# Performance work log

Measured on AMD Instinct MI355X. Metric: run time of the kernel, lower is better.

Reference implementation:

```python
import jax, jax.numpy as jnp
import numpy as np

EPS = 1e-5

def ln(x, g, b):
    m = x.mean(-1, keepdims=True)
    v = ((x - m) ** 2).mean(-1, keepdims=True)
    return (x - m) / jnp.sqrt(v + EPS) * g + b

def mha(x, in_w, in_b, out_w, out_b, nh):
    # Faithful nn.MultiheadAttention with batch_first=False: x is (L, B, D),
    # attention runs over axis 0 (sequence), axis 1 is batch.
    L, Bb, D = x.shape
    hd = D // nh
    qkv = x @ in_w.T + in_b                      # (L, B, 3D)
    q, k, v = jnp.split(qkv, 3, axis=-1)
    q = q.reshape(L, Bb, nh, hd) * (hd ** -0.5)
    k = k.reshape(L, Bb, nh, hd)
    v = v.reshape(L, Bb, nh, hd)
    a = jax.nn.softmax(jnp.einsum('lbhe,sbhe->bhls', q, k), axis=-1)
    o = jnp.einsum('bhls,sbhe->lbhe', a, v).reshape(L, Bb, D)
    return o @ out_w.T + out_b

def psb_forward(features, prev_slots,
                lnq_g, lnq_b, lnkv_g, lnkv_b,
                wq, wk, wv, wo,
                lnt_g, lnt_b, t_in_w, t_in_b, t_out_w, t_out_b,
                lno_g, lno_b, o_in_w, o_in_b, o_out_w, o_out_b,
                lnp_g, lnp_b, w1, b1, w2, b2):
    B, T, L, D = features.shape
    N = prev_slots.shape[2]
    nh = 1                                        # inverse_nh
    hd = D // nh
    slots = ln(prev_slots, lnq_g, lnq_b).reshape(B * T, N, D)
    xkv = ln(features, lnkv_g, lnkv_b).reshape(B * T, L, D)
    # ---- inverse cross attention (softmax over query/slot dim, renorm over keys) ----
    q = (slots @ wq.T).reshape(B * T, N, nh, hd).transpose(0, 2, 1, 3) * (D ** -0.5)
    k = (xkv @ wk.T).reshape(B * T, L, nh, hd).transpose(0, 2, 1, 3)
    v = (xkv @ wv.T).reshape(B * T, L, nh, hd).transpose(0, 2, 1, 3)
    attn = jnp.einsum('bhnd,bhsd->bhns', q, k)    # (BT, nh, N, L)
    attn = jax.nn.softmax(attn, axis=-2)          # over slots (queries)
    attn = attn / attn.sum(-1, keepdims=True)     # renormalize over keys
    s = jnp.einsum('bhns,bhsd->bnhd', attn, v).reshape(B * T, N, D) @ wo.T
    # ---- time attention: input (B*T, N, D); seq axis 0 = B*T, batch = N ----
    s = ln(s, lnt_g, lnt_b)
    s = mha(s, t_in_w, t_in_b, t_out_w, t_out_b, 4)
    # rearrange '(b t) n d -> (b n) t d'
    s = s.reshape(B, T, N, D).transpose(0, 2, 1, 3).reshape(B * N, T, D)
    # ---- object attention: seq axis 0 = B*N, batch = T ----
    s = ln(s, lno_g, lno_b)
    s = mha(s, o_in_w, o_in_b, o_out_w, o_out_b, 4)
    # faithful to torch .view(B, T, N, D) on a contiguous (B*N, T, D) tensor:
    # raw row-major reinterpretation (same as torch)
    s = s.reshape(B, T, N, D)
    # ---- FFN projection + residual with prev_slots ----
    s = ln(s, lnp_g, lnp_b)
    s = jax.nn.relu(s @ w1.T + b1) @ w2.T + b2
    return s + prev_slots

def setup_inputs() -> dict:
    key = jax.random.key(0)
    ks = jax.random.split(key, 16)
    B, T, L, D, N, F = 8, 16, 1024, 192, 8, 512
    w = lambda k, shape: jax.random.normal(k, shape, jnp.float32) * 0.02
    return {
        'features': jax.random.normal(ks[0], (B, T, L, D), jnp.float32),
        'prev_slots': jax.random.normal(ks[1], (B, T, N, D), jnp.float32),
        'lnq_g': jnp.ones((D,), jnp.float32), 'lnq_b': jnp.zeros((D,), jnp.float32),
        'lnkv_g': jnp.ones((D,), jnp.float32), 'lnkv_b': jnp.zeros((D,), jnp.float32),
        'wq': w(ks[2], (D, D)), 'wk': w(ks[3], (D, D)),
        'wv': w(ks[4], (D, D)), 'wo': w(ks[5], (D, D)),
        'lnt_g': jnp.ones((D,), jnp.float32), 'lnt_b': jnp.zeros((D,), jnp.float32),
        't_in_w': w(ks[6], (3 * D, D)), 't_in_b': jnp.zeros((3 * D,), jnp.float32),
        't_out_w': w(ks[7], (D, D)), 't_out_b': jnp.zeros((D,), jnp.float32),
        'lno_g': jnp.ones((D,), jnp.float32), 'lno_b': jnp.zeros((D,), jnp.float32),
        'o_in_w': w(ks[8], (3 * D, D)), 'o_in_b': jnp.zeros((3 * D,), jnp.float32),
        'o_out_w': w(ks[9], (D, D)), 'o_out_b': jnp.zeros((D,), jnp.float32),
        'lnp_g': jnp.ones((D,), jnp.float32), 'lnp_b': jnp.zeros((D,), jnp.float32),
        'w1': w(ks[10], (F, D)), 'b1': jnp.zeros((F,), jnp.float32),
        'w2': w(ks[11], (D, F)), 'b2': jnp.zeros((D,), jnp.float32),
    }

def reference(features, prev_slots,
              lnq_g, lnq_b, lnkv_g, lnkv_b,
              wq, wk, wv, wo,
              lnt_g, lnt_b, t_in_w, t_in_b, t_out_w, t_out_b,
              lno_g, lno_b, o_in_w, o_in_b, o_out_w, o_out_b,
              lnp_g, lnp_b, w1, b1, w2, b2):
    return psb_forward(features, prev_slots,
                       lnq_g, lnq_b, lnkv_g, lnkv_b,
                       wq, wk, wv, wo,
                       lnt_g, lnt_b, t_in_w, t_in_b, t_out_w, t_out_b,
                       lno_g, lno_b, o_in_w, o_in_b, o_out_w, o_out_b,
                       lnp_g, lnp_b, w1, b1, w2, b2)
```

## Files before the change

kernel.cpp:

```cpp
#include <hip/hip_runtime.h>
#include <hip/hip_bf16.h>
#include <stdint.h>

typedef __hip_bfloat16 bf16;

__device__ __forceinline__ float b2f(bf16 x){ return __bfloat162float(x); }
__device__ __forceinline__ bf16  f2b(float x){ return __float2bfloat16(x); }
__device__ __forceinline__ float bfl(unsigned u){ return __uint_as_float(u << 16); }
__device__ __forceinline__ float bfh(unsigned u){ return __uint_as_float(u & 0xffff0000u); }
__device__ __forceinline__ int dflag(const void* rawg){
  return *(const uint32_t*)rawg == 0x3F803F80u;
}

struct Ptrs26 { const void* p[26]; };
__global__ __launch_bounds__(256) void k_convert(Ptrs26 ps, float* __restrict__ dst){
  constexpr int kN[26] = {192,192,192,192, 36864,36864,36864,36864, 192,192,
                          110592,576, 36864,192, 192,192, 110592,576, 36864,192,
                          192,192, 98304,512, 98304,192};
  constexpr int kR[26] = {0,0,0,0, 0,0,0,0, 0,0,
                          576,0, 192,0, 0,0, 576,0, 192,0,
                          0,0, 512,0, 192,0};
  const int b = blockIdx.x;
  int tz = 0, boff = 0, off = 0;
  for (int i = 0; i < 26; ++i){
    const int nb = (kN[i] + 255) >> 8;
    if (b < boff + nb){ tz = i; break; }
    boff += nb; off += kN[i];
  }
  const int cnt = kN[tz];
  const int tid = (b - boff)*256 + threadIdx.x;
  if (tid >= cnt) return;
  const int flag = dflag(ps.p[0]);
  float v = flag ? b2f(((const bf16*)ps.p[tz])[tid]) : ((const float*)ps.p[tz])[tid];
  const int R = kR[tz];
  if (R == 0){
    dst[off + tid] = v;
  } else {
    const int K = cnt / R;
    int o = tid / K, e = tid - o*K;
    dst[off + e*R + o] = v;
  }
}

__global__ __launch_bounds__(192) void k_m1m2(
    const float* __restrict__ wq, const float* __restrict__ wk,
    const float* __restrict__ wo, const float* __restrict__ wv,
    const float* __restrict__ bkv,
    float* __restrict__ M1, float* __restrict__ M2t, float* __restrict__ cM2)
{
  __shared__ float sred[3];
  const int t = threadIdx.x, row = blockIdx.x, mat = blockIdx.y;
  float acc = 0.f;
  if (mat == 0){
    for (int d = 0; d < 192; ++d) acc += wq[d*192 + row] * wk[d*192 + t];
    M1[row*192 + t] = acc * 0.07216878364870323f;
  } else {
    for (int d = 0; d < 192; ++d) acc += wo[row*192 + d] * wv[d*192 + t];
    M2t[t*192 + row] = acc;
    float c = acc * bkv[t];
    #pragma unroll
    for (int o = 32; o > 0; o >>= 1) c += __shfl_xor(c, o);
    if ((t & 63) == 0) sred[t >> 6] = c;
    __syncthreads();
    if (t == 0) cM2[row] = sred[0] + sred[1] + sred[2];
  }
}

__global__ __launch_bounds__(192) void k_qprime(
    const void* __restrict__ prev, const void* __restrict__ rawg,
    const float* __restrict__ g, const float* __restrict__ be,
    const float* __restrict__ gkv, const float* __restrict__ bkv,
    const float* __restrict__ M1, float* __restrict__ Qg, float* __restrict__ cS)
{
  __shared__ float sRaw[8][196];
  __shared__ float sS[8][196];
  __shared__ float sMS[8][2];
  __shared__ float sCred[3][8];
  const int t = threadIdx.x, bt = blockIdx.x;
  const int flag = dflag(rawg);
  #pragma unroll
  for (int r = 0; r < 8; ++r){
    size_t idx = ((size_t)bt*8 + r)*192 + t;
    sRaw[r][t] = flag ? b2f(((const bf16*)prev)[idx]) : ((const float*)prev)[idx];
  }
  __syncthreads();
  if (t < 8){
    float s = 0.f, q = 0.f;
    for (int e = 0; e < 192; ++e){ float x = sRaw[t][e]; s += x; q += x*x; }
    float m = s*(1.f/192.f);
    float rstd = rsqrtf(q*(1.f/192.f) - m*m + 1e-5f);
    sMS[t][0] = m; sMS[t][1] = rstd;
  }
  __syncthreads();
  const float gg = g[t], bb = be[t];
  #pragma unroll
  for (int r = 0; r < 8; ++r)
    sS[r][t] = (sRaw[r][t] - sMS[r][0])*sMS[r][1]*gg + bb;
  __syncthreads();
  float acc[8] = {};
  for (int f = 0; f < 192; ++f){
    float mv = M1[f*192 + t];
    #pragma unroll
    for (int n = 0; n < 8; ++n) acc[n] += sS[n][f]*mv;
  }
  const float gk = gkv[t], bk = bkv[t];
  float c[8];
  #pragma unroll
  for (int n = 0; n < 8; ++n) c[n] = acc[n]*bk;
  #pragma unroll
  for (int o = 32; o > 0; o >>= 1){
    #pragma unroll
    for (int n = 0; n < 8; ++n) c[n] += __shfl_xor(c[n], o);
  }
  if ((t & 63) == 0){
    #pragma unroll
    for (int n = 0; n < 8; ++n) sCred[t >> 6][n] = c[n];
  }
  #pragma unroll
  for (int n = 0; n < 8; ++n) Qg[(size_t)bt*1536 + n*192 + t] = acc[n]*gk;
  __syncthreads();
  if (t < 8) cS[(size_t)bt*8 + t] = sCred[0][t] + sCred[1][t] + sCred[2][t];
}

__global__ __launch_bounds__(256) void k_front(
    const void* __restrict__ feat, const void* __restrict__ rawg,
    const float* __restrict__ Qg, const float* __restrict__ cSg,
    float* __restrict__ pP, float* __restrict__ pR)
{
  __shared__ float sX[16][196];
  __shared__ float sQ[8][196];
  __shared__ float sA[16][12];
  __shared__ float sRS[4][8];
  __shared__ float sCS[8];
  const int t = threadIdx.x, lane = t & 63, w = t >> 6;
  const int split = blockIdx.x, bt = blockIdx.y;
  const int flag = dflag(rawg);
  const int grp = lane >> 4;
  const int gl  = lane & 15;
  const int lrow = w*4 + grp;
  const int le0  = gl*12;
  const int pc = t >> 3, pn = t & 7;
  const size_t rowbase = (size_t)bt*1024 + (size_t)split*64;

  float4 pf0, pf1, pf2;
  uint2  pb0, pb1, pb2;

  auto issue = [&](int tile){
    size_t ro = (rowbase + (size_t)(tile*16 + lrow))*192 + le0;
    if (flag){
      const uint2* p2 = (const uint2*)((const bf16*)feat + ro);
      pb0 = p2[0]; pb1 = p2[1]; pb2 = p2[2];
    } else {
      const float4* p4 = (const float4*)((const float*)feat + ro);
      pf0 = p4[0]; pf1 = p4[1]; pf2 = p4[2];
    }
  };
  issue(0);

  for (int i = t; i < 1536; i += 256){
    int n = i / 192, e = i - n*192;
    sQ[n][e] = Qg[(size_t)bt*1536 + i];
  }
  if (t < 8) sCS[t] = cSg[(size_t)bt*8 + t];

  float accP[8] = {0,0,0,0,0,0,0,0};
  float rs[8]   = {0,0,0,0,0,0,0,0};
  __syncthreads();

  for (int tile = 0; tile < 4; ++tile){
    float x[12];
    if (flag){
      x[0]=bfl(pb0.x); x[1]=bfh(pb0.x); x[2]=bfl(pb0.y); x[3]=bfh(pb0.y);
      x[4]=bfl(pb1.x); x[5]=bfh(pb1.x); x[6]=bfl(pb1.y); x[7]=bfh(pb1.y);
      x[8]=bfl(pb2.x); x[9]=bfh(pb2.x); x[10]=bfl(pb2.y); x[11]=bfh(pb2.y);
    } else {
      x[0]=pf0.x; x[1]=pf0.y; x[2]=pf0.z; x[3]=pf0.w;
      x[4]=pf1.x; x[5]=pf1.y; x[6]=pf1.z; x[7]=pf1.w;
      x[8]=pf2.x; x[9]=pf2.y; x[10]=pf2.z; x[11]=pf2.w;
    }
    float s = 0.f, q = 0.f;
    #pragma unroll
    for (int j = 0; j < 12; ++j){ s += x[j]; q += x[j]*x[j]; }
    #pragma unroll
    for (int o = 1; o < 16; o <<= 1){ s += __shfl_xor(s, o); q += __shfl_xor(q, o); }
    float m = s*(1.f/192.f);
    float rstd = rsqrtf(q*(1.f/192.f) - m*m + 1e-5f);
    *(float4*)&sX[lrow][le0]   = make_float4((x[0]-m)*rstd,(x[1]-m)*rstd,(x[2]-m)*rstd,(x[3]-m)*rstd);
    *(float4*)&sX[lrow][le0+4] = make_float4((x[4]-m)*rstd,(x[5]-m)*rstd,(x[6]-m)*rstd,(x[7]-m)*rstd);
    *(float4*)&sX[lrow][le0+8] = make_float4((x[8]-m)*rstd,(x[9]-m)*rstd,(x[10]-m)*rstd,(x[11]-m)*rstd);
    if (tile < 3) issue(tile + 1);
    __syncthreads();

    float4 xa = *(const float4*)&sX[lrow][le0];
    float4 xb = *(const float4*)&sX[lrow][le0+4];
    float4 xc = *(const float4*)&sX[lrow][le0+8];
    float p[8];
    #pragma unroll
    for (int n = 0; n < 8; ++n){
      const float* qr = &sQ[n][le0];
      float4 qa = *(const float4*)qr;
      float4 qb = *(const float4*)(qr+4);
      float4 qc = *(const float4*)(qr+8);
      p[n] = xa.x*qa.x + xa.y*qa.y + xa.z*qa.z + xa.w*qa.w
           + xb.x*qb.x + xb.y*qb.y + xb.z*qb.z + xb.w*qb.w
           + xc.x*qc.x + xc.y*qc.y + xc.z*qc.z + xc.w*qc.w;
    }
    #pragma unroll
    for (int o = 1; o < 16; o <<= 1){
      #pragma unroll
      for (int n = 0; n < 8; ++n) p[n] += __shfl_xor(p[n], o);
    }
    #pragma unroll
    for (int n = 0; n < 8; ++n) p[n] += sCS[n];
    float mx = p[0];
    #pragma unroll
    for (int n = 1; n < 8; ++n) mx = fmaxf(mx, p[n]);
    float sum = 0.f;
    #pragma unroll
    for (int n = 0; n < 8; ++n){ p[n] = __expf(p[n]-mx); sum += p[n]; }
    float inv = 1.f/sum;
    #pragma unroll
    for (int n = 0; n < 8; ++n) p[n] *= inv;
    if (gl == 0){
      *(float4*)&sA[lrow][0] = make_float4(p[0],p[1],p[2],p[3]);
      *(float4*)&sA[lrow][4] = make_float4(p[4],p[5],p[6],p[7]);
      #pragma unroll
      for (int n = 0; n < 8; ++n) rs[n] += p[n];
    }
    __syncthreads();

    if (t < 192){
      #pragma unroll 4
      for (int k2 = 0; k2 < 16; ++k2){
        float av = sA[k2][pn];
        const float* xp2 = &sX[k2][pc*8];
        float4 u0 = *(const float4*)(xp2);
        float4 u1 = *(const float4*)(xp2 + 4);
        accP[0] += av*u0.x; accP[1] += av*u0.y; accP[2] += av*u0.z; accP[3] += av*u0.w;
        accP[4] += av*u1.x; accP[5] += av*u1.y; accP[6] += av*u1.z; accP[7] += av*u1.w;
      }
    }
    __syncthreads();
  }

  if (t < 192){
    float* pp = pP + (((size_t)bt*16 + split)*8 + pn)*192 + pc*8;
    *(float4*)pp       = make_float4(accP[0],accP[1],accP[2],accP[3]);
    *(float4*)(pp + 4) = make_float4(accP[4],accP[5],accP[6],accP[7]);
  }
  #pragma unroll
  for (int n = 0; n < 8; ++n){
    rs[n] += __shfl_xor(rs[n], 16);
    rs[n] += __shfl_xor(rs[n], 32);
  }
  if (lane == 0){
    *(float4*)&sRS[w][0] = make_float4(rs[0],rs[1],rs[2],rs[3]);
    *(float4*)&sRS[w][4] = make_float4(rs[4],rs[5],rs[6],rs[7]);
  }
  __syncthreads();
  if (t < 8) pR[((size_t)bt*16 + split)*8 + t] = sRS[0][t]+sRS[1][t]+sRS[2][t]+sRS[3][t];
}

__global__ __launch_bounds__(256) void k_finln(
    const float* __restrict__ pP, const float* __restrict__ pR, const float* __restrict__ M2t,
    const float* __restrict__ gkv, const float* __restrict__ cM2,
    const float* __restrict__ g, const float* __restrict__ be,
    const float* __restrict__ Wt, const float* __restrict__ bias, float* __restrict__ out)
{
  __shared__ float sP[2][196];
  __shared__ float sx[2][196];
  __shared__ float sInv[2];
  __shared__ float sredS[2][4], sredQ[2][4];
  const int t = threadIdx.x, lane = t & 63, w = t >> 6;
  const int r0 = blockIdx.x*2;
  const int bt = r0 >> 3;
  for (int j = t; j < 384; j += 256){
    int rr = (j >= 192) ? 1 : 0;
    int e = j - rr*192;
    int n = (r0 + rr) & 7;
    const float* src = pP + (((size_t)bt*16)*8 + n)*192 + e;
    float v = 0.f;
    #pragma unroll
    for (int s = 0; s < 16; ++s) v += src[(size_t)s*1536];
    sP[rr][e] = gkv[e] * v;
  }
  if (t < 2){
    int n = (r0 + t) & 7;
    float r = 0.f;
    #pragma unroll
    for (int s = 0; s < 16; ++s) r += pR[((size_t)bt*16 + s)*8 + n];
    sInv[t] = 1.f/r;
  }
  __syncthreads();
  float a0 = 0.f, a1 = 0.f;
  if (t < 192){
    for (int e = 0; e < 192; ++e){
      float wv = M2t[e*192 + t];
      a0 += sP[0][e]*wv; a1 += sP[1][e]*wv;
    }
    const float cm = cM2[t];
    a0 = a0*sInv[0] + cm; a1 = a1*sInv[1] + cm;
    float s0 = a0, q0 = a0*a0, s1 = a1, q1 = a1*a1;
    #pragma unroll
    for (int o = 32; o > 0; o >>= 1){
      s0 += __shfl_xor(s0,o); q0 += __shfl_xor(q0,o);
      s1 += __shfl_xor(s1,o); q1 += __shfl_xor(q1,o);
    }
    if (lane == 0){ sredS[0][w]=s0; sredQ[0][w]=q0; sredS[1][w]=s1; sredQ[1][w]=q1; }
  }
  __syncthreads();
  if (t < 192){
    float s0 = sredS[0][0]+sredS[0][1]+sredS[0][2];
    float q0 = sredQ[0][0]+sredQ[0][1]+sredQ[0][2];
    float s1 = sredS[1][0]+sredS[1][1]+sredS[1][2];
    float q1 = sredQ[1][0]+sredQ[1][1]+sredQ[1][2];
    float m0 = s0*(1.f/192.f), m1 = s1*(1.f/192.f);
    float r0s = rsqrtf(q0*(1.f/192.f) - m0*m0 + 1e-5f);
    float r1s = rsqrtf(q1*(1.f/192.f) - m1*m1 + 1e-5f);
    float gg = g[t], bb = be[t];
    sx[0][t] = (a0 - m0)*r0s*gg + bb;
    sx[1][t] = (a1 - m1)*r1s*gg + bb;
  }
  __syncthreads();
  if (t < 192){
    #pragma unroll
    for (int k = 0; k < 3; ++k){
      int o = t + k*192;
      float c0 = bias[o], c1 = bias[o];
      for (int e = 0; e < 192; ++e){
        float wv = Wt[e*576 + o];
        c0 += sx[0][e]*wv; c1 += sx[1][e]*wv;
      }
      out[(size_t)r0*576 + o] = c0;
      out[(size_t)(r0+1)*576 + o] = c1;
    }
  }
}

__global__ __launch_bounds__(256) void k_attn8(
    const float* __restrict__ qkv, float* __restrict__ ao, int S, int B)
{
  __shared__ float sK[128][52];
  __shared__ float sV[128][52];
  __shared__ float sQ[8][52];
  __shared__ float sS[8][132];
  const int t = threadIdx.x;
  const int qt = blockIdx.x, h = blockIdx.y, b = blockIdx.z;
  const float sc = 0.1443375673f;
  for (int i = t; i < S*12; i += 256){
    int ks = i / 12, c = i - ks*12;
    const float* base = qkv + ((size_t)ks*B + b)*576 + h*48 + c*4;
    *(float4*)&sK[ks][c*4] = *(const float4*)(base + 192);
    *(float4*)&sV[ks][c*4] = *(const float4*)(base + 384);
  }
  if (t < 96){
    int qr = t / 12, c = t - qr*12;
    int lq = qt*8 + qr;
    float4 qv = *(const float4*)(qkv + ((size_t)lq*B + b)*576 + h*48 + c*4);
    qv.x *= sc; qv.y *= sc; qv.z *= sc; qv.w *= sc;
    *(float4*)&sQ[qr][c*4] = qv;
  }
  __syncthreads();
  const int qr = t >> 5, kk = t & 31;
  for (int ks = kk; ks < S; ks += 32){
    float acc = 0.f;
    #pragma unroll
    for (int j = 0; j < 12; ++j){
      float4 qv = *(const float4*)&sQ[qr][j*4];
      float4 kv = *(const float4*)&sK[ks][j*4];
      acc += qv.x*kv.x + qv.y*kv.y + qv.z*kv.z + qv.w*kv.w;
    }
    sS[qr][ks] = acc;
  }
  float mx = -1e30f;
  for (int ks = kk; ks < S; ks += 32) mx = fmaxf(mx, sS[qr][ks]);
  #pragma unroll
  for (int m = 1; m < 32; m <<= 1) mx = fmaxf(mx, __shfl_xor(mx, m));
  float sum = 0.f;
  for (int ks = kk; ks < S; ks += 32){
    float e = __expf(sS[qr][ks] - mx);
    sS[qr][ks] = e;
    sum += e;
  }
  #pragma unroll
  for (int m = 1; m < 32; m <<= 1) sum += __shfl_xor(sum, m);
  const float inv = 1.f / sum;
  __syncthreads();
  const int d0 = (kk & 15)*3;
  float a0 = 0.f, a1 = 0.f, a2 = 0.f;
  for (int ks = (kk >> 4); ks < S; ks += 2){
    float p = sS[qr][ks];
    a0 += p*sV[ks][d0]; a1 += p*sV[ks][d0+1]; a2 += p*sV[ks][d0+2];
  }
  a0 += __shfl_xor(a0, 16); a1 += __shfl_xor(a1, 16); a2 += __shfl_xor(a2, 16);
  if (kk < 16){
    const int lq = qt*8 + qr;
    float* op = ao + ((size_t)lq*B + b)*192 + h*48 + d0;
    op[0] = a0*inv; op[1] = a1*inv; op[2] = a2*inv;
  }
}

__global__ __launch_bounds__(256) void k_projln(
    const float* __restrict__ aoT, const float* __restrict__ W1t, const float* __restrict__ b1v,
    const float* __restrict__ g, const float* __restrict__ be,
    const float* __restrict__ Wt, const float* __restrict__ bias, float* __restrict__ out)
{
  __shared__ float sin[2][196];
  __shared__ float sx[2][196];
  __shared__ float sredS[2][4], sredQ[2][4];
  const int t = threadIdx.x, lane = t & 63, w = t >> 6;
  const int r0 = blockIdx.x*2;
  if (t < 192){
    #pragma unroll
    for (int rr = 0; rr < 2; ++rr){
      int r = r0 + rr;
      int ls = r >> 4, tb = r & 15;
      int inrow = ((ls>>3)*16 + tb)*8 + (ls&7);
      sin[rr][t] = aoT[(size_t)inrow*192 + t];
    }
  }
  __syncthreads();
  float a0 = 0.f, a1 = 0.f;
  if (t < 192){
    a0 = b1v[t]; a1 = b1v[t];
    for (int e = 0; e < 192; ++e){
      float wv = W1t[e*192 + t];
      a0 += sin[0][e]*wv; a1 += sin[1][e]*wv;
    }
    float s0 = a0, q0 = a0*a0, s1 = a1, q1 = a1*a1;
    #pragma unroll
    for (int o = 32; o > 0; o >>= 1){
      s0 += __shfl_xor(s0,o); q0 += __shfl_xor(q0,o);
      s1 += __shfl_xor(s1,o); q1 += __shfl_xor(q1,o);
    }
    if (lane == 0){ sredS[0][w]=s0; sredQ[0][w]=q0; sredS[1][w]=s1; sredQ[1][w]=q1; }
  }
  __syncthreads();
  if (t < 192){
    float s0 = sredS[0][0]+sredS[0][1]+sredS[0][2];
    float q0 = sredQ[0][0]+sredQ[0][1]+sredQ[0][2];
    float s1 = sredS[1][0]+sredS[1][1]+sredS[1][2];
    float q1 = sredQ[1][0]+sredQ[1][1]+sredQ[1][2];
    float m0 = s0*(1.f/192.f), m1 = s1*(1.f/192.f);
    float r0s = rsqrtf(q0*(1.f/192.f) - m0*m0 + 1e-5f);
    float r1s = rsqrtf(q1*(1.f/192.f) - m1*m1 + 1e-5f);
    float gg = g[t], bb = be[t];
    sx[0][t] = (a0 - m0)*r0s*gg + bb;
    sx[1][t] = (a1 - m1)*r1s*gg + bb;
  }
  __syncthreads();
  if (t < 192){
    #pragma unroll
    for (int k = 0; k < 3; ++k){
      int o = t + k*192;
      float c0 = bias[o], c1 = bias[o];
      for (int e = 0; e < 192; ++e){
        float wv = Wt[e*576 + o];
        c0 += sx[0][e]*wv; c1 += sx[1][e]*wv;
      }
      out[(size_t)r0*576 + o] = c0;
      out[(size_t)(r0+1)*576 + o] = c1;
    }
  }
}

__global__ __launch_bounds__(256) void k_ffn2(
    const float* __restrict__ aoO, const float* __restrict__ Wpt, const float* __restrict__ bp,
    const float* __restrict__ g, const float* __restrict__ be,
    const float* __restrict__ w1t, const float* __restrict__ b1,
    const float* __restrict__ w2t, const float* __restrict__ b2,
    const void* __restrict__ prev, const void* __restrict__ rawg, void* __restrict__ out)
{
  __shared__ float sin[2][196];
  __shared__ float sx[2][196];
  __shared__ float sh[2][512];
  __shared__ float sredS[2][4], sredQ[2][4];
  const int t = threadIdx.x, lane = t & 63, w = t >> 6;
  const int r0 = blockIdx.x*2;
  const int flag = dflag(rawg);
  if (t < 192){
    sin[0][t] = aoO[(size_t)r0*192 + t];
    sin[1][t] = aoO[(size_t)(r0+1)*192 + t];
  }
  __syncthreads();
  float a0 = 0.f, a1 = 0.f;
  if (t < 192){
    a0 = bp[t]; a1 = bp[t];
    for (int e = 0; e < 192; ++e){
      float wv = Wpt[e*192 + t];
      a0 += sin[0][e]*wv; a1 += sin[1][e]*wv;
    }
    float s0 = a0, q0 = a0*a0, s1 = a1, q1 = a1*a1;
    #pragma unroll
    for (int o = 32; o > 0; o >>= 1){
      s0 += __shfl_xor(s0,o); q0 += __shfl_xor(q0,o);
      s1 += __shfl_xor(s1,o); q1 += __shfl_xor(q1,o);
    }
    if (lane == 0){ sredS[0][w]=s0; sredQ[0][w]=q0; sredS[1][w]=s1; sredQ[1][w]=q1; }
  }
  __syncthreads();
  if (t < 192){
    float s0 = sredS[0][0]+sredS[0][1]+sredS[0][2];
    float q0 = sredQ[0][0]+sredQ[0][1]+sredQ[0][2];
    float s1 = sredS[1][0]+sredS[1][1]+sredS[1][2];
    float q1 = sredQ[1][0]+sredQ[1][1]+sredQ[1][2];
    float m0 = s0*(1.f/192.f), m1 = s1*(1.f/192.f);
    float r0s = rsqrtf(q0*(1.f/192.f) - m0*m0 + 1e-5f);
    float r1s = rsqrtf(q1*(1.f/192.f) - m1*m1 + 1e-5f);
    float gg = g[t], bb = be[t];
    sx[0][t] = (a0 - m0)*r0s*gg + bb;
    sx[1][t] = (a1 - m1)*r1s*gg + bb;
  }
  __syncthreads();
  float h0[2], h1[2];
  {
    float ba = b1[t], bb2v = b1[t+256];
    #pragma unroll
    for (int r = 0; r < 2; ++r){ h0[r]=ba; h1[r]=bb2v; }
  }
  for (int e = 0; e < 192; ++e){
    const float* wr = w1t + e*512;
    float wa = wr[t], wb = wr[t+256];
    #pragma unroll
    for (int r = 0; r < 2; ++r){
      float xv = sx[r][e];
      h0[r] += xv*wa; h1[r] += xv*wb;
    }
  }
  #pragma unroll
  for (int r = 0; r < 2; ++r){
    sh[r][t]     = fmaxf(h0[r], 0.f);
    sh[r][t+256] = fmaxf(h1[r], 0.f);
  }
  __syncthreads();
  if (t < 192){
    float acc[2];
    float bb3 = b2[t];
    acc[0] = bb3; acc[1] = bb3;
    for (int e = 0; e < 512; ++e){
      float wv = w2t[e*192 + t];
      acc[0] += sh[0][e]*wv; acc[1] += sh[1][e]*wv;
    }
    #pragma unroll
    for (int r = 0; r < 2; ++r){
      size_t oi = (size_t)(r0+r)*192 + t;
      float res = flag ? b2f(((const bf16*)prev)[oi]) : ((const float*)prev)[oi];
      float y = acc[r] + res;
      if (flag) ((bf16*)out)[oi] = f2b(y);
      else      ((float*)out)[oi] = y;
    }
  }
}

extern "C" void kernel_launch(void* const* d_in, const int* in_sizes, int n_in,
                              void* d_out, int out_size, void* d_ws, size_t ws_size,
                              hipStream_t stream)
{
  const void* feat = d_in[0];
  const void* prev = d_in[1];
  const void* rawg = d_in[2];
  static const int kWN[26] = {192,192,192,192, 36864,36864,36864,36864, 192,192,
                              110592,576, 36864,192, 192,192, 110592,576, 36864,192,
                              192,192, 98304,512, 98304,192};
  Ptrs26 ps;
  for (int i = 0; i < 26; ++i) ps.p[i] = d_in[2 + i];

  float* wconv = (float*)d_ws;
  size_t woff[26]; size_t acc_ = 0;
  for (int i = 0; i < 26; ++i){ woff[i] = acc_; acc_ += kWN[i]; }
  float* M1   = wconv + 643136;
  float* M2t  = M1 + 36864;
  float* Qp   = M2t + 36864;
  float* pP   = Qp + 196608;
  float* pR   = pP + 3145728;
  float* qkvT = pR + 16384;
  float* aoT  = qkvT + 589824;
  float* qkvO = aoT + 196608;
  float* aoO  = qkvO + 589824;
  const size_t needed = (size_t)((char*)(aoO + 196608) - (char*)d_ws);
  if (ws_size < needed) return;
  float* cM2 = qkvO;
  float* cS  = aoO;

  const float* c_lnq_g  = wconv + woff[0];
  const float* c_lnq_b  = wconv + woff[1];
  const float* c_lnkv_g = wconv + woff[2];
  const float* c_lnkv_b = wconv + woff[3];
  const float* c_wq     = wconv + woff[4];
  const float* c_wk     = wconv + woff[5];
  const float* c_wv     = wconv + woff[6];
  const float* c_wo     = wconv + woff[7];
  const float* c_lnt_g  = wconv + woff[8];
  const float* c_lnt_b  = wconv + woff[9];
  const float* c_tin_w  = wconv + woff[10];
  const float* c_tin_b  = wconv + woff[11];
  const float* c_tout_w = wconv + woff[12];
  const float* c_tout_b = wconv + woff[13];
  const float* c_lno_g  = wconv + woff[14];
  const float* c_lno_b  = wconv + woff[15];
  const float* c_oin_w  = wconv + woff[16];
  const float* c_oin_b  = wconv + woff[17];
  const float* c_oout_w = wconv + woff[18];
  const float* c_oout_b = wconv + woff[19];
  const float* c_lnp_g  = wconv + woff[20];
  const float* c_lnp_b  = wconv + woff[21];
  const float* c_w1     = wconv + woff[22];
  const float* c_b1     = wconv + woff[23];
  const float* c_w2     = wconv + woff[24];
  const float* c_b2     = wconv + woff[25];

  k_convert<<<2517, 256, 0, stream>>>(ps, wconv);
  k_m1m2<<<dim3(192, 2), 192, 0, stream>>>(c_wq, c_wk, c_wo, c_wv, c_lnkv_b, M1, M2t, cM2);
  k_qprime<<<128, 192, 0, stream>>>(prev, rawg, c_lnq_g, c_lnq_b, c_lnkv_g, c_lnkv_b,
                                    M1, Qp, cS);
  k_front<<<dim3(16, 128), 256, 0, stream>>>(feat, rawg, Qp, cS, pP, pR);
  k_finln<<<512, 256, 0, stream>>>(pP, pR, M2t, c_lnkv_g, cM2, c_lnt_g, c_lnt_b,
                                   c_tin_w, c_tin_b, qkvT);
  k_attn8<<<dim3(16,4,8), 256, 0, stream>>>(qkvT, aoT, 128, 8);
  k_projln<<<512, 256, 0, stream>>>(aoT, c_tout_w, c_tout_b, c_lno_g, c_lno_b,
                                    c_oin_w, c_oin_b, qkvO);
  k_attn8<<<dim3(8,4,16), 256, 0, stream>>>(qkvO, aoO, 64, 16);
  k_ffn2<<<512, 256, 0, stream>>>(aoO, c_oout_w, c_oout_b, c_lnp_g, c_lnp_b,
                                  c_w1, c_b1, c_w2, c_b2, prev, rawg, d_out);
}
```

Measured before the change: 364.9 us.

## Accumulate attention-weighted features in registers instead of shared-memory tiles in k_front

The front kernel no longer stages normalized feature rows and attention weights in shared memory with two barriers per tile. Each thread keeps its 12 normalized elements and accumulates all 8 slot outer products in 96 registers, then reduces across lane groups with shuffles and across waves through a shared buffer at the end. The next tile's load is issued earlier and launch bounds request two blocks per CU. This removes per-tile syncs and LDS traffic but raises register pressure heavily, which may cause spills or lower occupancy.

```diff
diff --git a/kernel.cpp b/kernel.cpp
--- a/kernel.cpp
+++ b/kernel.cpp
@@ -122,16 +122,14 @@
   if (t < 8) cS[(size_t)bt*8 + t] = sCred[0][t] + sCred[1][t] + sCred[2][t];
 }
 
-__global__ __launch_bounds__(256) void k_front(
+__global__ __launch_bounds__(256, 2) void k_front(
     const void* __restrict__ feat, const void* __restrict__ rawg,
     const float* __restrict__ Qg, const float* __restrict__ cSg,
     float* __restrict__ pP, float* __restrict__ pR)
 {
-  __shared__ float sX[16][196];
   __shared__ float sQ[8][196];
-  __shared__ float sA[16][12];
+  __shared__ float sR[4][16][100];
   __shared__ float sRS[4][8];
-  __shared__ float sCS[8];
   const int t = threadIdx.x, lane = t & 63, w = t >> 6;
   const int split = blockIdx.x, bt = blockIdx.y;
   const int flag = dflag(rawg);
@@ -139,7 +137,6 @@
   const int gl  = lane & 15;
   const int lrow = w*4 + grp;
   const int le0  = gl*12;
-  const int pc = t >> 3, pn = t & 7;
   const size_t rowbase = (size_t)bt*1024 + (size_t)split*64;
 
   float4 pf0, pf1, pf2;
@@ -161,10 +158,14 @@
     int n = i / 192, e = i - n*192;
     sQ[n][e] = Qg[(size_t)bt*1536 + i];
   }
-  if (t < 8) sCS[t] = cSg[(size_t)bt*8 + t];
-
-  float accP[8] = {0,0,0,0,0,0,0,0};
-  float rs[8]   = {0,0,0,0,0,0,0,0};
+  float cs[8];
+  #pragma unroll
+  for (int n = 0; n < 8; ++n) cs[n] = cSg[(size_t)bt*8 + n];
+
+  float accP[96];
+  #pragma unroll
+  for (int i = 0; i < 96; ++i) accP[i] = 0.f;
+  float rs[8] = {0,0,0,0,0,0,0,0};
   __syncthreads();
 
   for (int tile = 0; tile < 4; ++tile){
@@ -178,6 +179,7 @@
       x[4]=pf1.x; x[5]=pf1.y; x[6]=pf1.z; x[7]=pf1.w;
       x[8]=pf2.x; x[9]=pf2.y; x[10]=pf2.z; x[11]=pf2.w;
     }
+    if (tile < 3) issue(tile + 1);
     float s = 0.f, q = 0.f;
     #pragma unroll
     for (int j = 0; j < 12; ++j){ s += x[j]; q += x[j]*x[j]; }
@@ -185,15 +187,8 @@
     for (int o = 1; o < 16; o <<= 1){ s += __shfl_xor(s, o); q += __shfl_xor(q, o); }
     float m = s*(1.f/192.f);
     float rstd = rsqrtf(q*(1.f/192.f) - m*m + 1e-5f);
-    *(float4*)&sX[lrow][le0]   = make_float4((x[0]-m)*rstd,(x[1]-m)*rstd,(x[2]-m)*rstd,(x[3]-m)*rstd);
-    *(float4*)&sX[lrow][le0+4] = make_float4((x[4]-m)*rstd,(x[5]-m)*rstd,(x[6]-m)*rstd,(x[7]-m)*rstd);
-    *(float4*)&sX[lrow][le0+8] = make_float4((x[8]-m)*rstd,(x[9]-m)*rstd,(x[10]-m)*rstd,(x[11]-m)*rstd);
-    if (tile < 3) issue(tile + 1);
-    __syncthreads();
-
-    float4 xa = *(const float4*)&sX[lrow][le0];
-    float4 xb = *(const float4*)&sX[lrow][le0+4];
-    float4 xc = *(const float4*)&sX[lrow][le0+8];
+    #pragma unroll
+    for (int j = 0; j < 12; ++j) x[j] = (x[j]-m)*rstd;
     float p[8];
     #pragma unroll
     for (int n = 0; n < 8; ++n){
@@ -201,9 +196,9 @@
       float4 qa = *(const float4*)qr;
       float4 qb = *(const float4*)(qr+4);
       float4 qc = *(const float4*)(qr+8);
-      p[n] = xa.x*qa.x + xa.y*qa.y + xa.z*qa.z + xa.w*qa.w
-           + xb.x*qb.x + xb.y*qb.y + xb.z*qb.z + xb.w*qb.w
-           + xc.x*qc.x + xc.y*qc.y + xc.z*qc.z + xc.w*qc.w;
+      p[n] = x[0]*qa.x + x[1]*qa.y + x[2]*qa.z + x[3]*qa.w
+           + x[4]*qb.x + x[5]*qb.y + x[6]*qb.z + x[7]*qb.w
+           + x[8]*qc.x + x[9]*qc.y + x[10]*qc.z + x[11]*qc.w;
     }
     #pragma unroll
     for (int o = 1; o < 16; o <<= 1){
@@ -211,7 +206,7 @@
       for (int n = 0; n < 8; ++n) p[n] += __shfl_xor(p[n], o);
     }
     #pragma unroll
-    for (int n = 0; n < 8; ++n) p[n] += sCS[n];
+    for (int n = 0; n < 8; ++n) p[n] += cs[n];
     float mx = p[0];
     #pragma unroll
     for (int n = 1; n < 8; ++n) mx = fmaxf(mx, p[n]);
@@ -222,31 +217,25 @@
     #pragma unroll
     for (int n = 0; n < 8; ++n) p[n] *= inv;
     if (gl == 0){
-      *(float4*)&sA[lrow][0] = make_float4(p[0],p[1],p[2],p[3]);
-      *(float4*)&sA[lrow][4] = make_float4(p[4],p[5],p[6],p[7]);
       #pragma unroll
       for (int n = 0; n < 8; ++n) rs[n] += p[n];
     }
-    __syncthreads();
-
-    if (t < 192){
-      #pragma unroll 4
-      for (int k2 = 0; k2 < 16; ++k2){
-        float av = sA[k2][pn];
-        const float* xp2 = &sX[k2][pc*8];
-        float4 u0 = *(const float4*)(xp2);
-        float4 u1 = *(const float4*)(xp2 + 4);
-        accP[0] += av*u0.x; accP[1] += av*u0.y; accP[2] += av*u0.z; accP[3] += av*u0.w;
-        accP[4] += av*u1.x; accP[5] += av*u1.y; accP[6] += av*u1.z; accP[7] += av*u1.w;
-      }
-    }
-    __syncthreads();
-  }
-
-  if (t < 192){
-    float* pp = pP + (((size_t)bt*16 + split)*8 + pn)*192 + pc*8;
-    *(float4*)pp       = make_float4(accP[0],accP[1],accP[2],accP[3]);
-    *(float4*)(pp + 4) = make_float4(accP[4],accP[5],accP[6],accP[7]);
+    #pragma unroll
+    for (int n = 0; n < 8; ++n){
+      #pragma unroll
+      for (int j = 0; j < 12; ++j) accP[n*12+j] += p[n]*x[j];
+    }
+  }
+
+  #pragma unroll
+  for (int i = 0; i < 96; ++i){
+    accP[i] += __shfl_xor(accP[i], 16);
+    accP[i] += __shfl_xor(accP[i], 32);
+  }
+  if (grp == 0){
+    #pragma unroll
+    for (int i = 0; i < 96; i += 4)
+      *(float4*)&sR[w][gl][i] = make_float4(accP[i],accP[i+1],accP[i+2],accP[i+3]);
   }
   #pragma unroll
   for (int n = 0; n < 8; ++n){
@@ -258,6 +247,15 @@
     *(float4*)&sRS[w][4] = make_float4(rs[4],rs[5],rs[6],rs[7]);
   }
   __syncthreads();
+  if (t < 192){
+    const int gl2 = t/12, j2 = t - gl2*12;
+    #pragma unroll
+    for (int n = 0; n < 8; ++n){
+      const int o = n*12 + j2;
+      float v = sR[0][gl2][o] + sR[1][gl2][o] + sR[2][gl2][o] + sR[3][gl2][o];
+      pP[(((size_t)bt*16 + split)*8 + n)*192 + t] = v;
+    }
+  }
   if (t < 8) pR[((size_t)bt*16 + split)*8 + t] = sRS[0][t]+sRS[1][t]+sRS[2][t]+sRS[3][t];
 }
 
```

After: 377.4 us. 1.03x slower.

## Merge weight conversion with M1/M2 precompute and trim front-kernel barriers

Applied to the files above, without the earlier changes.

Folds the weight-conversion kernel and the M1/M2 folded-weight product kernel into one launch. The M1/M2 blocks read raw wq/wk/wv/wo directly, so those four matrices are no longer converted. In the front kernel, normalized features stay in registers for the slot-score dot product and are written to shared memory only afterwards, dropping one barrier per tile and issuing the next prefetch earlier. This removes a launch and some synchronization. In exchange the M1/M2 blocks run alongside conversion blocks that have a different shape, and a quarter of each M1/M2 block's threads sit idle.

```diff
diff --git a/kernel.cpp b/kernel.cpp
--- a/kernel.cpp
+++ b/kernel.cpp
@@ -13,54 +13,71 @@
 }
 
 struct Ptrs26 { const void* p[26]; };
-__global__ __launch_bounds__(256) void k_convert(Ptrs26 ps, float* __restrict__ dst){
+__global__ __launch_bounds__(256) void k_prep(Ptrs26 ps, float* __restrict__ dst,
+    float* __restrict__ M1, float* __restrict__ M2t, float* __restrict__ cM2)
+{
   constexpr int kN[26] = {192,192,192,192, 36864,36864,36864,36864, 192,192,
                           110592,576, 36864,192, 192,192, 110592,576, 36864,192,
                           192,192, 98304,512, 98304,192};
   constexpr int kR[26] = {0,0,0,0, 0,0,0,0, 0,0,
                           576,0, 192,0, 0,0, 576,0, 192,0,
                           0,0, 512,0, 192,0};
-  const int b = blockIdx.x;
-  int tz = 0, boff = 0, off = 0;
-  for (int i = 0; i < 26; ++i){
-    const int nb = (kN[i] + 255) >> 8;
-    if (b < boff + nb){ tz = i; break; }
-    boff += nb; off += kN[i];
-  }
-  const int cnt = kN[tz];
-  const int tid = (b - boff)*256 + threadIdx.x;
-  if (tid >= cnt) return;
+  const int b = blockIdx.x, t = threadIdx.x;
   const int flag = dflag(ps.p[0]);
-  float v = flag ? b2f(((const bf16*)ps.p[tz])[tid]) : ((const float*)ps.p[tz])[tid];
-  const int R = kR[tz];
-  if (R == 0){
-    dst[off + tid] = v;
-  } else {
-    const int K = cnt / R;
-    int o = tid / K, e = tid - o*K;
-    dst[off + e*R + o] = v;
-  }
-}
-
-__global__ __launch_bounds__(192) void k_m1m2(
-    const float* __restrict__ wq, const float* __restrict__ wk,
-    const float* __restrict__ wo, const float* __restrict__ wv,
-    const float* __restrict__ bkv,
-    float* __restrict__ M1, float* __restrict__ M2t, float* __restrict__ cM2)
-{
+  if (b < 1941){
+    int tz = 0, boff = 0, off = 0;
+    for (int i = 0; i < 26; ++i){
+      const int nb = (i >= 4 && i < 8) ? 0 : ((kN[i] + 255) >> 8);
+      if (b < boff + nb){ tz = i; break; }
+      boff += nb; off += kN[i];
+    }
+    const int cnt = kN[tz];
+    const int tid = (b - boff)*256 + t;
+    if (tid >= cnt) return;
+    float v = flag ? b2f(((const bf16*)ps.p[tz])[tid]) : ((const float*)ps.p[tz])[tid];
+    const int R = kR[tz];
+    if (R == 0){
+      dst[off + tid] = v;
+    } else {
+      const int K = cnt / R;
+      int o = tid / K, e = tid - o*K;
+      dst[off + e*R + o] = v;
+    }
+    return;
+  }
   __shared__ float sred[3];
-  const int t = threadIdx.x, row = blockIdx.x, mat = blockIdx.y;
+  const int bm = b - 1941;
+  const int mat = bm >= 192;
+  const int row = mat ? bm - 192 : bm;
   float acc = 0.f;
-  if (mat == 0){
-    for (int d = 0; d < 192; ++d) acc += wq[d*192 + row] * wk[d*192 + t];
-    M1[row*192 + t] = acc * 0.07216878364870323f;
-  } else {
-    for (int d = 0; d < 192; ++d) acc += wo[row*192 + d] * wv[d*192 + t];
-    M2t[t*192 + row] = acc;
-    float c = acc * bkv[t];
+  if (t < 192){
+    if (!mat){
+      if (flag){
+        const bf16* wq = (const bf16*)ps.p[4]; const bf16* wk = (const bf16*)ps.p[5];
+        for (int d = 0; d < 192; ++d) acc += b2f(wq[d*192 + row]) * b2f(wk[d*192 + t]);
+      } else {
+        const float* wq = (const float*)ps.p[4]; const float* wk = (const float*)ps.p[5];
+        for (int d = 0; d < 192; ++d) acc += wq[d*192 + row] * wk[d*192 + t];
+      }
+      M1[row*192 + t] = acc * 0.07216878364870323f;
+    } else {
+      if (flag){
+        const bf16* wo = (const bf16*)ps.p[7]; const bf16* wv = (const bf16*)ps.p[6];
+        for (int d = 0; d < 192; ++d) acc += b2f(wo[row*192 + d]) * b2f(wv[d*192 + t]);
+      } else {
+        const float* wo = (const float*)ps.p[7]; const float* wv = (const float*)ps.p[6];
+        for (int d = 0; d < 192; ++d) acc += wo[row*192 + d] * wv[d*192 + t];
+      }
+      M2t[t*192 + row] = acc;
+    }
+  }
+  if (mat){
+    float bk = 0.f;
+    if (t < 192) bk = flag ? b2f(((const bf16*)ps.p[3])[t]) : ((const float*)ps.p[3])[t];
+    float c = (t < 192) ? acc*bk : 0.f;
     #pragma unroll
     for (int o = 32; o > 0; o >>= 1) c += __shfl_xor(c, o);
-    if ((t & 63) == 0) sred[t >> 6] = c;
+    if ((t & 63) == 0 && t < 192) sred[t >> 6] = c;
     __syncthreads();
     if (t == 0) cM2[row] = sred[0] + sred[1] + sred[2];
   }
@@ -127,16 +144,15 @@
     const float* __restrict__ Qg, const float* __restrict__ cSg,
     float* __restrict__ pP, float* __restrict__ pR)
 {
-  __shared__ float sX[16][196];
   __shared__ float sQ[8][196];
-  __shared__ float sA[16][12];
+  __shared__ float sX[16][200];
+  __shared__ float sA[16][8];
   __shared__ float sRS[4][8];
   __shared__ float sCS[8];
   const int t = threadIdx.x, lane = t & 63, w = t >> 6;
   const int split = blockIdx.x, bt = blockIdx.y;
   const int flag = dflag(rawg);
-  const int grp = lane >> 4;
-  const int gl  = lane & 15;
+  const int grp = lane >> 4, gl = lane & 15;
   const int lrow = w*4 + grp;
   const int le0  = gl*12;
   const int pc = t >> 3, pn = t & 7;
@@ -144,7 +160,6 @@
 
   float4 pf0, pf1, pf2;
   uint2  pb0, pb1, pb2;
-
   auto issue = [&](int tile){
     size_t ro = (rowbase + (size_t)(tile*16 + lrow))*192 + le0;
     if (flag){
@@ -162,7 +177,6 @@
     sQ[n][e] = Qg[(size_t)bt*1536 + i];
   }
   if (t < 8) sCS[t] = cSg[(size_t)bt*8 + t];
-
   float accP[8] = {0,0,0,0,0,0,0,0};
   float rs[8]   = {0,0,0,0,0,0,0,0};
   __syncthreads();
@@ -178,6 +192,7 @@
       x[4]=pf1.x; x[5]=pf1.y; x[6]=pf1.z; x[7]=pf1.w;
       x[8]=pf2.x; x[9]=pf2.y; x[10]=pf2.z; x[11]=pf2.w;
     }
+    if (tile < 3) issue(tile + 1);
     float s = 0.f, q = 0.f;
     #pragma unroll
     for (int j = 0; j < 12; ++j){ s += x[j]; q += x[j]*x[j]; }
@@ -185,15 +200,8 @@
     for (int o = 1; o < 16; o <<= 1){ s += __shfl_xor(s, o); q += __shfl_xor(q, o); }
     float m = s*(1.f/192.f);
     float rstd = rsqrtf(q*(1.f/192.f) - m*m + 1e-5f);
-    *(float4*)&sX[lrow][le0]   = make_float4((x[0]-m)*rstd,(x[1]-m)*rstd,(x[2]-m)*rstd,(x[3]-m)*rstd);
-    *(float4*)&sX[lrow][le0+4] = make_float4((x[4]-m)*rstd,(x[5]-m)*rstd,(x[6]-m)*rstd,(x[7]-m)*rstd);
-    *(float4*)&sX[lrow][le0+8] = make_float4((x[8]-m)*rstd,(x[9]-m)*rstd,(x[10]-m)*rstd,(x[11]-m)*rstd);
-    if (tile < 3) issue(tile + 1);
-    __syncthreads();
-
-    float4 xa = *(const float4*)&sX[lrow][le0];
-    float4 xb = *(const float4*)&sX[lrow][le0+4];
-    float4 xc = *(const float4*)&sX[lrow][le0+8];
+    #pragma unroll
+    for (int j = 0; j < 12; ++j) x[j] = (x[j]-m)*rstd;
     float p[8];
     #pragma unroll
     for (int n = 0; n < 8; ++n){
@@ -201,9 +209,9 @@
       float4 qa = *(const float4*)qr;
       float4 qb = *(const float4*)(qr+4);
       float4 qc = *(const float4*)(qr+8);
-      p[n] = xa.x*qa.x + xa.y*qa.y + xa.z*qa.z + xa.w*qa.w
-           + xb.x*qb.x + xb.y*qb.y + xb.z*qb.z + xb.w*qb.w
-           + xc.x*qc.x + xc.y*qc.y + xc.z*qc.z + xc.w*qc.w;
+      p[n] = x[0]*qa.x + x[1]*qa.y + x[2]*qa.z + x[3]*qa.w
+           + x[4]*qb.x + x[5]*qb.y + x[6]*qb.z + x[7]*qb.w
+           + x[8]*qc.x + x[9]*qc.y + x[10]*qc.z + x[11]*qc.w;
     }
     #pragma unroll
     for (int o = 1; o < 16; o <<= 1){
@@ -221,6 +229,10 @@
     float inv = 1.f/sum;
     #pragma unroll
     for (int n = 0; n < 8; ++n) p[n] *= inv;
+    __syncthreads();
+    *(float4*)&sX[lrow][le0]   = make_float4(x[0],x[1],x[2],x[3]);
+    *(float4*)&sX[lrow][le0+4] = make_float4(x[4],x[5],x[6],x[7]);
+    *(float4*)&sX[lrow][le0+8] = make_float4(x[8],x[9],x[10],x[11]);
     if (gl == 0){
       *(float4*)&sA[lrow][0] = make_float4(p[0],p[1],p[2],p[3]);
       *(float4*)&sA[lrow][4] = make_float4(p[4],p[5],p[6],p[7]);
@@ -228,7 +240,6 @@
       for (int n = 0; n < 8; ++n) rs[n] += p[n];
     }
     __syncthreads();
-
     if (t < 192){
       #pragma unroll 4
       for (int k2 = 0; k2 < 16; ++k2){
@@ -240,7 +251,6 @@
         accP[4] += av*u1.x; accP[5] += av*u1.y; accP[6] += av*u1.z; accP[7] += av*u1.w;
       }
     }
-    __syncthreads();
   }
 
   if (t < 192){
@@ -586,10 +596,6 @@
   const float* c_lnq_b  = wconv + woff[1];
   const float* c_lnkv_g = wconv + woff[2];
   const float* c_lnkv_b = wconv + woff[3];
-  const float* c_wq     = wconv + woff[4];
-  const float* c_wk     = wconv + woff[5];
-  const float* c_wv     = wconv + woff[6];
-  const float* c_wo     = wconv + woff[7];
   const float* c_lnt_g  = wconv + woff[8];
   const float* c_lnt_b  = wconv + woff[9];
   const float* c_tin_w  = wconv + woff[10];
@@ -609,8 +615,7 @@
   const float* c_w2     = wconv + woff[24];
   const float* c_b2     = wconv + woff[25];
 
-  k_convert<<<2517, 256, 0, stream>>>(ps, wconv);
-  k_m1m2<<<dim3(192, 2), 192, 0, stream>>>(c_wq, c_wk, c_wo, c_wv, c_lnkv_b, M1, M2t, cM2);
+  k_prep<<<2325, 256, 0, stream>>>(ps, wconv, M1, M2t, cM2);
   k_qprime<<<128, 192, 0, stream>>>(prev, rawg, c_lnq_g, c_lnq_b, c_lnkv_g, c_lnkv_b,
                                     M1, Qp, cS);
   k_front<<<dim3(16, 128), 256, 0, stream>>>(feat, rawg, Qp, cS, pP, pR);
```

Measured after the change: 365.6 us. About the same (+0.2%).
